# Kernel tuning notes

Hardware: AMD Instinct MI355X
Metric: run time of the kernel (lower is better)

The kernel has to match this reference:

```python
import jax, jax.numpy as jnp
import numpy as np

D_MODEL = 1024
NUM_HEADS = 16
D_K = D_MODEL // NUM_HEADS


def setup_inputs() -> dict:
    key = jax.random.key(0)
    ks = jax.random.split(key, 9)
    s = 1.0 / np.sqrt(D_MODEL)
    return {
        "z": jax.random.normal(ks[0], (4, 2048, D_MODEL), dtype=jnp.float32),
        "Wq": jax.random.uniform(ks[1], (D_MODEL, D_MODEL), jnp.float32, -s, s),
        "bq": jax.random.uniform(ks[2], (D_MODEL,), jnp.float32, -s, s),
        "Wk": jax.random.uniform(ks[3], (D_MODEL, D_MODEL), jnp.float32, -s, s),
        "bk": jax.random.uniform(ks[4], (D_MODEL,), jnp.float32, -s, s),
        "Wv": jax.random.uniform(ks[5], (D_MODEL, D_MODEL), jnp.float32, -s, s),
        "bv": jax.random.uniform(ks[6], (D_MODEL,), jnp.float32, -s, s),
        "Wo": jax.random.uniform(ks[7], (D_MODEL, D_MODEL), jnp.float32, -s, s),
        "bo": jax.random.uniform(ks[8], (D_MODEL,), jnp.float32, -s, s),
    }


def reference(z, Wq, bq, Wk, bk, Wv, bv, Wo, bo):
    B, S, _ = z.shape
    # project and split heads: [B, H, S, d_k]
    def proj(W, b):
        return (z @ W.T + b).reshape(B, S, NUM_HEADS, D_K).transpose(0, 2, 1, 3)
    Q, K, V = proj(Wq, bq), proj(Wk, bk), proj(Wv, bv)
    scale = 1.0 / np.sqrt(D_K)
    scores = jnp.einsum('bhqd,bhkd->bhqk', Q, K) * scale
    probs = jax.nn.softmax(scores, axis=-1)
    ctx = jnp.einsum('bhqk,bhkd->bhqd', probs, V)
    ctx = ctx.transpose(0, 2, 1, 3).reshape(B, S, D_MODEL)
    return ctx @ Wo.T + bo
```

## Files before the change

### kernel.cpp

```cpp
#include <hip/hip_runtime.h>
#include <stdint.h>

#define D_MODEL 1024
#define NHEAD 16
#define DKH 64
#define BATCH 4
#define SEQ 2048
#define M_ROWS (BATCH*SEQ)
#define NBH (BATCH*NHEAD)

typedef float f32x4 __attribute__((ext_vector_type(4)));
typedef float f32x16 __attribute__((ext_vector_type(16)));
typedef __bf16 bf16x8 __attribute__((ext_vector_type(8)));
typedef __bf16 bf16x4v __attribute__((ext_vector_type(4)));
typedef short short4v __attribute__((ext_vector_type(4)));
typedef unsigned int uint2v __attribute__((ext_vector_type(2)));

__device__ __forceinline__ unsigned short f2bf(float x) {
    __bf16 b = (__bf16)x;
    return __builtin_bit_cast(unsigned short, b);
}

#define GLL(gsrc, ldst) \
    __builtin_amdgcn_global_load_lds((const __attribute__((address_space(1))) void*)(gsrc), \
                                     (__attribute__((address_space(3))) void*)(ldst), 16, 0, 0)

__global__ __launch_bounds__(256) void k_convert(
    const float* __restrict__ z,  const float* __restrict__ wq,
    const float* __restrict__ wk, const float* __restrict__ wv,
    const float* __restrict__ wo,
    const float* __restrict__ bq, const float* __restrict__ bk,
    const float* __restrict__ bv,
    unsigned short* __restrict__ zb, unsigned short* __restrict__ wqkv,
    unsigned short* __restrict__ wob, float* __restrict__ biasf)
{
    int i = blockIdx.x * 256 + threadIdx.x;
    {
        float4 v = ((const float4*)z)[i];
        ushort4 o; o.x = f2bf(v.x); o.y = f2bf(v.y); o.z = f2bf(v.z); o.w = f2bf(v.w);
        ((ushort4*)zb)[i] = o;
    }
    if (i < 262144) {
        float4 v;
        ushort4 o;
        v = ((const float4*)wq)[i];
        o.x=f2bf(v.x); o.y=f2bf(v.y); o.z=f2bf(v.z); o.w=f2bf(v.w);
        ((ushort4*)wqkv)[i] = o;
        v = ((const float4*)wk)[i];
        o.x=f2bf(v.x); o.y=f2bf(v.y); o.z=f2bf(v.z); o.w=f2bf(v.w);
        ((ushort4*)wqkv)[262144 + i] = o;
        v = ((const float4*)wv)[i];
        o.x=f2bf(v.x); o.y=f2bf(v.y); o.z=f2bf(v.z); o.w=f2bf(v.w);
        ((ushort4*)wqkv)[524288 + i] = o;
        v = ((const float4*)wo)[i];
        o.x=f2bf(v.x); o.y=f2bf(v.y); o.z=f2bf(v.z); o.w=f2bf(v.w);
        ((ushort4*)wob)[i] = o;
    }
    if (i < 1024) {
        biasf[i]        = bq[i];
        biasf[1024 + i] = bk[i];
        biasf[2048 + i] = bv[i];
    }
}

__global__ __launch_bounds__(256) void k_gemm_qkv(
    const unsigned short* __restrict__ A,
    const unsigned short* __restrict__ Bw,
    const float* __restrict__ biasf,
    unsigned short* __restrict__ qb, unsigned short* __restrict__ kb,
    unsigned short* __restrict__ vtb)
{
    __shared__ unsigned short lds_a[128 * 32];
    __shared__ unsigned short lds_b[128 * 32];

    const int NT = 3072 / 128;
    int bid = blockIdx.x;
    int tn = bid % NT, tm = bid / NT;
    int m0 = tm * 128, n0 = tn * 128;
    int tid = threadIdx.x, wid = tid >> 6, lane = tid & 63;
    int wm = wid >> 1, wn = wid & 1;

    f32x4 acc[4][4] = {};

    int srow = lane >> 2;
    int scol = (lane & 3) * 8;

    for (int kt = 0; kt < 32; ++kt) {
        int k0 = kt * 32;
#pragma unroll
        for (int i = 0; i < 2; ++i) {
            int rb = (wid * 2 + i) * 16;
            GLL(A  + (size_t)(m0 + rb + srow) * 1024 + k0 + scol, lds_a + rb * 32);
            GLL(Bw + (size_t)(n0 + rb + srow) * 1024 + k0 + scol, lds_b + rb * 32);
        }
        __syncthreads();
        bf16x8 af[4], bfr[4];
#pragma unroll
        for (int i = 0; i < 4; ++i)
            af[i] = *(const bf16x8*)(lds_a + (wm * 64 + i * 16 + (lane & 15)) * 32 + (lane >> 4) * 8);
#pragma unroll
        for (int j = 0; j < 4; ++j)
            bfr[j] = *(const bf16x8*)(lds_b + (wn * 64 + j * 16 + (lane & 15)) * 32 + (lane >> 4) * 8);
#pragma unroll
        for (int i = 0; i < 4; ++i)
#pragma unroll
            for (int j = 0; j < 4; ++j)
                acc[i][j] = __builtin_amdgcn_mfma_f32_16x16x32_bf16(af[i], bfr[j], acc[i][j], 0, 0, 0);
        __syncthreads();
    }

    const float QSC = 0.18033688011112042f;
    int t = n0 >> 10;
#pragma unroll
    for (int j = 0; j < 4; ++j) {
        int col = n0 + wn * 64 + j * 16 + (lane & 15);
        float bias = biasf[col];
        int d  = col & 1023;
        int h  = d >> 6;
        int dk = d & 63;
#pragma unroll
        for (int i = 0; i < 4; ++i) {
#pragma unroll
            for (int r = 0; r < 4; ++r) {
                int row = m0 + wm * 64 + i * 16 + (lane >> 4) * 4 + r;
                float v = acc[i][j][r] + bias;
                if (t == 0) v *= QSC;
                unsigned short bv16 = f2bf(v);
                int b_ = row >> 11, s_ = row & 2047;
                int bh = b_ * NHEAD + h;
                if (t == 0) {
                    qb[((size_t)bh * SEQ + s_) * DKH + dk] = bv16;
                } else if (t == 1) {
                    int kvblk = s_ >> 6, r64 = s_ & 63;
                    int t32 = r64 >> 5, l5 = r64 & 31;
                    int ds = dk >> 4, hi2 = (dk >> 3) & 1, e = dk & 7;
                    kb[((size_t)(bh * 32 + kvblk)) * 4096 +
                       (t32 * 4 + ds) * 512 + (hi2 * 32 + l5) * 8 + e] = bv16;
                } else {
                    int kvblk = s_ >> 6, kv64 = s_ & 63;
                    int ks = kv64 >> 3, hi2 = (kv64 >> 2) & 1, e = kv64 & 3;
                    int vt = dk >> 5, l5 = dk & 31;
                    vtb[((size_t)(bh * 32 + kvblk)) * 4096 +
                        (vt * 8 + ks) * 256 + (hi2 * 32 + l5) * 4 + e] = bv16;
                }
            }
        }
    }
}

__global__ __launch_bounds__(512) void k_attn(
    const unsigned short* __restrict__ qg,
    const unsigned short* __restrict__ kb,
    const unsigned short* __restrict__ vtb,
    unsigned short* __restrict__ ctxb)
{
    __shared__ unsigned short lds_k[2][4096];
    __shared__ unsigned short lds_v[2][4096];

    int bid = blockIdx.x;
    int x = bid & 7, li = bid >> 3;
    int bh = x * 8 + (li >> 3);
    int qt = li & 7;

    int tid = threadIdx.x, wid = tid >> 6, lane = tid & 63;
    int lq = lane & 31, hi = lane >> 5;

    bf16x8 aq[4];
    {
        const unsigned short* qp = qg + ((size_t)bh * SEQ + qt * 256 + wid * 32 + lq) * DKH + hi * 8;
#pragma unroll
        for (int d = 0; d < 4; ++d) aq[d] = *(const bf16x8*)(qp + d * 16);
    }

    float lsum = 0.f;
    f32x16 oa0 = {};
    f32x16 oa1 = {};

    const unsigned short* kbase = kb  + (size_t)bh * 32 * 4096;
    const unsigned short* vbase = vtb + (size_t)bh * 32 * 4096;
    int so = wid * 512 + lane * 8;

    GLL(kbase + so, &lds_k[0][wid * 512]);
    GLL(vbase + so, &lds_v[0][wid * 512]);
    asm volatile("s_waitcnt vmcnt(0)" ::: "memory");
    __builtin_amdgcn_s_barrier();

    for (int kt = 0; kt < 32; ++kt) {
        int cur = kt & 1;
        if (kt < 31) {
            GLL(kbase + (size_t)(kt + 1) * 4096 + so, &lds_k[cur ^ 1][wid * 512]);
            GLL(vbase + (size_t)(kt + 1) * 4096 + so, &lds_v[cur ^ 1][wid * 512]);
        }

        f32x16 st0 = {}, st1 = {};
        __builtin_amdgcn_s_setprio(1);
#pragma unroll
        for (int ds = 0; ds < 4; ++ds) {
            bf16x8 kf0 = *(const bf16x8*)(&lds_k[cur][(ds)     * 512 + lane * 8]);
            bf16x8 kf1 = *(const bf16x8*)(&lds_k[cur][(4 + ds) * 512 + lane * 8]);
            st0 = __builtin_amdgcn_mfma_f32_32x32x16_bf16(kf0, aq[ds], st0, 0, 0, 0);
            st1 = __builtin_amdgcn_mfma_f32_32x32x16_bf16(kf1, aq[ds], st1, 0, 0, 0);
        }
        __builtin_amdgcn_s_setprio(0);

        short4v w[8];
#pragma unroll
        for (int ks = 0; ks < 4; ++ks) {
            {
                float p0 = __builtin_amdgcn_exp2f(st0[4 * ks + 0]);
                float p1 = __builtin_amdgcn_exp2f(st0[4 * ks + 1]);
                float p2 = __builtin_amdgcn_exp2f(st0[4 * ks + 2]);
                float p3 = __builtin_amdgcn_exp2f(st0[4 * ks + 3]);
                lsum += (p0 + p1) + (p2 + p3);
                bf16x4v pb;
                pb[0] = (__bf16)p0; pb[1] = (__bf16)p1; pb[2] = (__bf16)p2; pb[3] = (__bf16)p3;
                w[ks] = __builtin_bit_cast(short4v, pb);
            }
            {
                float p0 = __builtin_amdgcn_exp2f(st1[4 * ks + 0]);
                float p1 = __builtin_amdgcn_exp2f(st1[4 * ks + 1]);
                float p2 = __builtin_amdgcn_exp2f(st1[4 * ks + 2]);
                float p3 = __builtin_amdgcn_exp2f(st1[4 * ks + 3]);
                lsum += (p0 + p1) + (p2 + p3);
                bf16x4v pb;
                pb[0] = (__bf16)p0; pb[1] = (__bf16)p1; pb[2] = (__bf16)p2; pb[3] = (__bf16)p3;
                w[4 + ks] = __builtin_bit_cast(short4v, pb);
            }
        }

        __builtin_amdgcn_s_setprio(1);
#pragma unroll
        for (int ks = 0; ks < 8; ++ks) {
            short4v vf0 = *(const short4v*)(&lds_v[cur][(ks)     * 256 + lane * 4]);
            short4v vf1 = *(const short4v*)(&lds_v[cur][(8 + ks) * 256 + lane * 4]);
            oa0 = __builtin_amdgcn_mfma_f32_32x32x8bf16_1k(vf0, w[ks], oa0, 0, 0, 0);
            oa1 = __builtin_amdgcn_mfma_f32_32x32x8bf16_1k(vf1, w[ks], oa1, 0, 0, 0);
        }
        __builtin_amdgcn_s_setprio(0);

        if (kt < 31) {
            asm volatile("s_waitcnt vmcnt(0)" ::: "memory");
            __builtin_amdgcn_sched_barrier(0);
            __builtin_amdgcn_s_barrier();
        }
    }

    int b_ = bh >> 4, h = bh & 15;
    lsum += __shfl_xor(lsum, 32);
    float inv = 1.0f / lsum;
    int s_ = qt * 256 + wid * 32 + lq;
    unsigned short* op = ctxb + (((size_t)b_ * SEQ + s_) * NHEAD + h) * DKH;
#pragma unroll
    for (int m = 0; m < 4; ++m) {
        {
            unsigned int u0 = ((unsigned int)f2bf(oa0[4 * m + 1] * inv) << 16) | f2bf(oa0[4 * m + 0] * inv);
            unsigned int u1 = ((unsigned int)f2bf(oa0[4 * m + 3] * inv) << 16) | f2bf(oa0[4 * m + 2] * inv);
            *(uint2v*)(op + 8 * m + 4 * hi) = (uint2v){ u0, u1 };
        }
        {
            unsigned int u0 = ((unsigned int)f2bf(oa1[4 * m + 1] * inv) << 16) | f2bf(oa1[4 * m + 0] * inv);
            unsigned int u1 = ((unsigned int)f2bf(oa1[4 * m + 3] * inv) << 16) | f2bf(oa1[4 * m + 2] * inv);
            *(uint2v*)(op + 32 + 8 * m + 4 * hi) = (uint2v){ u0, u1 };
        }
    }
}

__global__ __launch_bounds__(256) void k_gemm_out(
    const unsigned short* __restrict__ A,
    const unsigned short* __restrict__ Bw,
    const float* __restrict__ bo,
    float* __restrict__ out)
{
    __shared__ unsigned short lds_a[128 * 32];
    __shared__ unsigned short lds_b[128 * 32];

    const int NT = 1024 / 128;
    int bid = blockIdx.x;
    int tn = bid % NT, tm = bid / NT;
    int m0 = tm * 128, n0 = tn * 128;
    int tid = threadIdx.x, wid = tid >> 6, lane = tid & 63;
    int wm = wid >> 1, wn = wid & 1;

    f32x4 acc[4][4] = {};

    int srow = lane >> 2;
    int scol = (lane & 3) * 8;

    for (int kt = 0; kt < 32; ++kt) {
        int k0 = kt * 32;
#pragma unroll
        for (int i = 0; i < 2; ++i) {
            int rb = (wid * 2 + i) * 16;
            GLL(A  + (size_t)(m0 + rb + srow) * 1024 + k0 + scol, lds_a + rb * 32);
            GLL(Bw + (size_t)(n0 + rb + srow) * 1024 + k0 + scol, lds_b + rb * 32);
        }
        __syncthreads();
        bf16x8 af[4], bfr[4];
#pragma unroll
        for (int i = 0; i < 4; ++i)
            af[i] = *(const bf16x8*)(lds_a + (wm * 64 + i * 16 + (lane & 15)) * 32 + (lane >> 4) * 8);
#pragma unroll
        for (int j = 0; j < 4; ++j)
            bfr[j] = *(const bf16x8*)(lds_b + (wn * 64 + j * 16 + (lane & 15)) * 32 + (lane >> 4) * 8);
#pragma unroll
        for (int i = 0; i < 4; ++i)
#pragma unroll
            for (int j = 0; j < 4; ++j)
                acc[i][j] = __builtin_amdgcn_mfma_f32_16x16x32_bf16(af[i], bfr[j], acc[i][j], 0, 0, 0);
        __syncthreads();
    }

#pragma unroll
    for (int j = 0; j < 4; ++j) {
        int col = n0 + wn * 64 + j * 16 + (lane & 15);
        float bias = bo[col];
#pragma unroll
        for (int i = 0; i < 4; ++i) {
#pragma unroll
            for (int r = 0; r < 4; ++r) {
                int row = m0 + wm * 64 + i * 16 + (lane >> 4) * 4 + r;
                out[(size_t)row * 1024 + col] = acc[i][j][r] + bias;
            }
        }
    }
}

extern "C" void kernel_launch(void* const* d_in, const int* in_sizes, int n_in,
                              void* d_out, int out_size, void* d_ws, size_t ws_size,
                              hipStream_t stream)
{
    const float* z  = (const float*)d_in[0];
    const float* Wq = (const float*)d_in[1];
    const float* bq = (const float*)d_in[2];
    const float* Wk = (const float*)d_in[3];
    const float* bk = (const float*)d_in[4];
    const float* Wv = (const float*)d_in[5];
    const float* bv = (const float*)d_in[6];
    const float* Wo = (const float*)d_in[7];
    const float* bo = (const float*)d_in[8];
    float* out = (float*)d_out;

    char* ws = (char*)d_ws;
    unsigned short* zb   = (unsigned short*)(ws);
    unsigned short* ctxb = (unsigned short*)(ws);
    unsigned short* wqkv = (unsigned short*)(ws + (16ull << 20));
    unsigned short* wob  = (unsigned short*)(ws + (22ull << 20));
    float*          biasf= (float*)(ws + (24ull << 20));
    unsigned short* qb   = (unsigned short*)(ws + (25ull << 20));
    unsigned short* kb   = (unsigned short*)(ws + (41ull << 20));
    unsigned short* vtb  = (unsigned short*)(ws + (57ull << 20));

    k_convert<<<8192, 256, 0, stream>>>(z, Wq, Wk, Wv, Wo, bq, bk, bv, zb, wqkv, wob, biasf);
    k_gemm_qkv<<<64 * 24, 256, 0, stream>>>(zb, wqkv, biasf, qb, kb, vtb);
    k_attn<<<NBH * 8, 512, 0, stream>>>(qb, kb, vtb, ctxb);
    k_gemm_out<<<64 * 8, 256, 0, stream>>>(ctxb, wob, bo, out);
}
```

Before: 227.4 us.

## Software-pipeline attention loop: overlap previous tile's PV MMA with next QK and softmax

Restructures the attention inner loop so each step computes QK^T for tile t while running the PV MFMAs for tile t-1, using double-buffered probability registers (wA/wB). K and V loads are staggered by one tile, with a final PV epilogue. The goal is to keep the matrix units busy during exp2/convert work and to hide LDS latency by interleaving independent MFMA chains. In exchange it raises register pressure from the extra probability buffer and interleaved fragments, which could lower occupancy or cause spills.

```diff
diff --git a/kernel.cpp b/kernel.cpp
--- a/kernel.cpp
+++ b/kernel.cpp
@@ -148,6 +148,59 @@
     }
 }
 
+
+#define ATTN_STEP(LDSK, LDSV, WPREV, WCUR, DO_PV)                                   \
+    {                                                                               \
+        f32x16 st0 = {}, st1 = {};                                                  \
+        __builtin_amdgcn_s_setprio(1);                                              \
+        _Pragma("unroll")                                                           \
+        for (int ds = 0; ds < 4; ++ds) {                                            \
+            bf16x8 kf0 = *(const bf16x8*)(&(LDSK)[(ds) * 512 + lane * 8]);          \
+            bf16x8 kf1 = *(const bf16x8*)(&(LDSK)[(4 + ds) * 512 + lane * 8]);      \
+            st0 = __builtin_amdgcn_mfma_f32_32x32x16_bf16(kf0, aq[ds], st0, 0, 0, 0); \
+            st1 = __builtin_amdgcn_mfma_f32_32x32x16_bf16(kf1, aq[ds], st1, 0, 0, 0); \
+            if (DO_PV) {                                                            \
+                short4v vf0 = *(const short4v*)(&(LDSV)[(2 * ds) * 256 + lane * 4]);        \
+                short4v vf1 = *(const short4v*)(&(LDSV)[(8 + 2 * ds) * 256 + lane * 4]);    \
+                oa0 = __builtin_amdgcn_mfma_f32_32x32x8bf16_1k(vf0, WPREV[2 * ds], oa0, 0, 0, 0); \
+                oa1 = __builtin_amdgcn_mfma_f32_32x32x8bf16_1k(vf1, WPREV[2 * ds], oa1, 0, 0, 0); \
+                short4v vf2 = *(const short4v*)(&(LDSV)[(2 * ds + 1) * 256 + lane * 4]);    \
+                short4v vf3 = *(const short4v*)(&(LDSV)[(8 + 2 * ds + 1) * 256 + lane * 4]);\
+                oa0 = __builtin_amdgcn_mfma_f32_32x32x8bf16_1k(vf2, WPREV[2 * ds + 1], oa0, 0, 0, 0); \
+                oa1 = __builtin_amdgcn_mfma_f32_32x32x8bf16_1k(vf3, WPREV[2 * ds + 1], oa1, 0, 0, 0); \
+            }                                                                       \
+        }                                                                           \
+        __builtin_amdgcn_s_setprio(0);                                              \
+        _Pragma("unroll")                                                           \
+        for (int ks = 0; ks < 4; ++ks) {                                            \
+            {                                                                       \
+                float p0 = __builtin_amdgcn_exp2f(st0[4 * ks + 0]);                 \
+                float p1 = __builtin_amdgcn_exp2f(st0[4 * ks + 1]);                 \
+                float p2 = __builtin_amdgcn_exp2f(st0[4 * ks + 2]);                 \
+                float p3 = __builtin_amdgcn_exp2f(st0[4 * ks + 3]);                 \
+                lsum += (p0 + p1) + (p2 + p3);                                      \
+                bf16x4v pb;                                                         \
+                pb[0] = (__bf16)p0; pb[1] = (__bf16)p1; pb[2] = (__bf16)p2; pb[3] = (__bf16)p3; \
+                WCUR[ks] = __builtin_bit_cast(short4v, pb);                         \
+            }                                                                       \
+            {                                                                       \
+                float p0 = __builtin_amdgcn_exp2f(st1[4 * ks + 0]);                 \
+                float p1 = __builtin_amdgcn_exp2f(st1[4 * ks + 1]);                 \
+                float p2 = __builtin_amdgcn_exp2f(st1[4 * ks + 2]);                 \
+                float p3 = __builtin_amdgcn_exp2f(st1[4 * ks + 3]);                 \
+                lsum += (p0 + p1) + (p2 + p3);                                      \
+                bf16x4v pb;                                                         \
+                pb[0] = (__bf16)p0; pb[1] = (__bf16)p1; pb[2] = (__bf16)p2; pb[3] = (__bf16)p3; \
+                WCUR[4 + ks] = __builtin_bit_cast(short4v, pb);                     \
+            }                                                                       \
+        }                                                                           \
+    }
+
+#define DRAIN_BARRIER()                                         \
+    asm volatile("s_waitcnt vmcnt(0)" ::: "memory");            \
+    __builtin_amdgcn_sched_barrier(0);                          \
+    __builtin_amdgcn_s_barrier();
+
 __global__ __launch_bounds__(512) void k_attn(
     const unsigned short* __restrict__ qg,
     const unsigned short* __restrict__ kb,
@@ -175,75 +228,48 @@
     float lsum = 0.f;
     f32x16 oa0 = {};
     f32x16 oa1 = {};
+    short4v wA[8], wB[8];
 
     const unsigned short* kbase = kb  + (size_t)bh * 32 * 4096;
     const unsigned short* vbase = vtb + (size_t)bh * 32 * 4096;
     int so = wid * 512 + lane * 8;
-
-    GLL(kbase + so, &lds_k[0][wid * 512]);
-    GLL(vbase + so, &lds_v[0][wid * 512]);
-    asm volatile("s_waitcnt vmcnt(0)" ::: "memory");
-    __builtin_amdgcn_s_barrier();
-
-    for (int kt = 0; kt < 32; ++kt) {
-        int cur = kt & 1;
-        if (kt < 31) {
-            GLL(kbase + (size_t)(kt + 1) * 4096 + so, &lds_k[cur ^ 1][wid * 512]);
-            GLL(vbase + (size_t)(kt + 1) * 4096 + so, &lds_v[cur ^ 1][wid * 512]);
-        }
-
-        f32x16 st0 = {}, st1 = {};
-        __builtin_amdgcn_s_setprio(1);
-#pragma unroll
-        for (int ds = 0; ds < 4; ++ds) {
-            bf16x8 kf0 = *(const bf16x8*)(&lds_k[cur][(ds)     * 512 + lane * 8]);
-            bf16x8 kf1 = *(const bf16x8*)(&lds_k[cur][(4 + ds) * 512 + lane * 8]);
-            st0 = __builtin_amdgcn_mfma_f32_32x32x16_bf16(kf0, aq[ds], st0, 0, 0, 0);
-            st1 = __builtin_amdgcn_mfma_f32_32x32x16_bf16(kf1, aq[ds], st1, 0, 0, 0);
-        }
-        __builtin_amdgcn_s_setprio(0);
-
-        short4v w[8];
-#pragma unroll
-        for (int ks = 0; ks < 4; ++ks) {
-            {
-                float p0 = __builtin_amdgcn_exp2f(st0[4 * ks + 0]);
-                float p1 = __builtin_amdgcn_exp2f(st0[4 * ks + 1]);
-                float p2 = __builtin_amdgcn_exp2f(st0[4 * ks + 2]);
-                float p3 = __builtin_amdgcn_exp2f(st0[4 * ks + 3]);
-                lsum += (p0 + p1) + (p2 + p3);
-                bf16x4v pb;
-                pb[0] = (__bf16)p0; pb[1] = (__bf16)p1; pb[2] = (__bf16)p2; pb[3] = (__bf16)p3;
-                w[ks] = __builtin_bit_cast(short4v, pb);
-            }
-            {
-                float p0 = __builtin_amdgcn_exp2f(st1[4 * ks + 0]);
-                float p1 = __builtin_amdgcn_exp2f(st1[4 * ks + 1]);
-                float p2 = __builtin_amdgcn_exp2f(st1[4 * ks + 2]);
-                float p3 = __builtin_amdgcn_exp2f(st1[4 * ks + 3]);
-                lsum += (p0 + p1) + (p2 + p3);
-                bf16x4v pb;
-                pb[0] = (__bf16)p0; pb[1] = (__bf16)p1; pb[2] = (__bf16)p2; pb[3] = (__bf16)p3;
-                w[4 + ks] = __builtin_bit_cast(short4v, pb);
-            }
-        }
-
-        __builtin_amdgcn_s_setprio(1);
-#pragma unroll
-        for (int ks = 0; ks < 8; ++ks) {
-            short4v vf0 = *(const short4v*)(&lds_v[cur][(ks)     * 256 + lane * 4]);
-            short4v vf1 = *(const short4v*)(&lds_v[cur][(8 + ks) * 256 + lane * 4]);
-            oa0 = __builtin_amdgcn_mfma_f32_32x32x8bf16_1k(vf0, w[ks], oa0, 0, 0, 0);
-            oa1 = __builtin_amdgcn_mfma_f32_32x32x8bf16_1k(vf1, w[ks], oa1, 0, 0, 0);
-        }
-        __builtin_amdgcn_s_setprio(0);
-
-        if (kt < 31) {
-            asm volatile("s_waitcnt vmcnt(0)" ::: "memory");
-            __builtin_amdgcn_sched_barrier(0);
-            __builtin_amdgcn_s_barrier();
-        }
-    }
+    unsigned short* ldk0 = &lds_k[0][wid * 512];
+    unsigned short* ldk1 = &lds_k[1][wid * 512];
+    unsigned short* ldv0 = &lds_v[0][wid * 512];
+    unsigned short* ldv1 = &lds_v[1][wid * 512];
+
+    GLL(kbase + so, ldk0);
+    DRAIN_BARRIER();
+
+    GLL(kbase + 4096 + so, ldk1);
+    GLL(vbase + so, ldv0);
+    ATTN_STEP(lds_k[0], lds_v[0], wB, wA, false);
+    DRAIN_BARRIER();
+
+    for (int t = 1; t < 31; t += 2) {
+        GLL(kbase + (size_t)(t + 1) * 4096 + so, ldk0);
+        GLL(vbase + (size_t)t * 4096 + so, ldv1);
+        ATTN_STEP(lds_k[1], lds_v[0], wA, wB, true);
+        DRAIN_BARRIER();
+        if (t + 2 < 32) GLL(kbase + (size_t)(t + 2) * 4096 + so, ldk1);
+        GLL(vbase + (size_t)(t + 1) * 4096 + so, ldv0);
+        ATTN_STEP(lds_k[0], lds_v[1], wB, wA, true);
+        DRAIN_BARRIER();
+    }
+
+    GLL(vbase + (size_t)31 * 4096 + so, ldv1);
+    ATTN_STEP(lds_k[1], lds_v[0], wA, wB, true);
+    DRAIN_BARRIER();
+
+    __builtin_amdgcn_s_setprio(1);
+#pragma unroll
+    for (int ks = 0; ks < 8; ++ks) {
+        short4v vf0 = *(const short4v*)(&lds_v[1][(ks) * 256 + lane * 4]);
+        short4v vf1 = *(const short4v*)(&lds_v[1][(8 + ks) * 256 + lane * 4]);
+        oa0 = __builtin_amdgcn_mfma_f32_32x32x8bf16_1k(vf0, wB[ks], oa0, 0, 0, 0);
+        oa1 = __builtin_amdgcn_mfma_f32_32x32x8bf16_1k(vf1, wB[ks], oa1, 0, 0, 0);
+    }
+    __builtin_amdgcn_s_setprio(0);
 
     int b_ = bh >> 4, h = bh & 15;
     lsum += __shfl_xor(lsum, 32);
```

New measurement: 223.3 us. Within noise of the previous version (-1.8%).
